# Kernel optimization log

Measured on AMD Instinct MI355X. Metric: run time of the kernel, lower is better.

## Reference

```python
import jax, jax.numpy as jnp
import numpy as np

D_MODEL = 256; H = 8; D_FF = 1024; BLOCKS = 2
NUM_ITEMS = 200000; NUM_USERS = 100000; T_DLT = 512
B = 256; INTER = 50; INTRA = 20; CAND = 2048
NEG_INF = -1e9

def layer_norm(x, g, b, eps=1e-6):
    m = x.mean(-1, keepdims=True)
    s = x.std(-1, keepdims=True, ddof=1)  # torch .std is unbiased
    return g * (x - m) / (s + eps) + b

def pos_encoding(L, d):
    pos = jnp.arange(L, dtype=jnp.float32)[:, None]
    div = jnp.exp(jnp.arange(0, d, 2, dtype=jnp.float32) * (-jnp.log(10000.0) / d))
    pe = jnp.zeros((L, d), dtype=jnp.float32)
    pe = pe.at[:, 0::2].set(jnp.sin(pos * div))
    pe = pe.at[:, 1::2].set(jnp.cos(pos * div))
    return pe

def setup_inputs() -> dict:
    key = jax.random.key(0)
    ks = jax.random.split(key, 20)
    d = D_MODEL
    w = lambda k, shape, s: jax.random.normal(k, shape, dtype=jnp.float32) * s
    s = 1.0 / np.sqrt(d)
    inp = {}
    inp["item_emb"] = w(ks[0], (NUM_ITEMS, d), 0.02)
    inp["user_emb"] = w(ks[1], (NUM_USERS, d), 0.02)
    inp["time_emb"] = w(ks[2], (T_DLT, d), 0.02)
    inp["Wq"] = w(ks[3], (d, d), s); inp["bq"] = jnp.zeros((d,), jnp.float32)
    inp["Wk"] = w(ks[4], (d, d), s); inp["bk"] = jnp.zeros((d,), jnp.float32)
    inp["Wv"] = w(ks[5], (d, d), s); inp["bv"] = jnp.zeros((d,), jnp.float32)
    inp["Wo"] = w(ks[6], (d, d), s); inp["bo"] = jnp.zeros((d,), jnp.float32)
    inp["ln1_g"] = jnp.ones((d,), jnp.float32); inp["ln1_b"] = jnp.zeros((d,), jnp.float32)
    inp["W1"] = w(ks[7], (d, D_FF), s); inp["b1"] = jnp.zeros((D_FF,), jnp.float32)
    inp["W2"] = w(ks[8], (D_FF, d), 1.0 / np.sqrt(D_FF)); inp["b2"] = jnp.zeros((d,), jnp.float32)
    inp["ln2_g"] = jnp.ones((d,), jnp.float32); inp["ln2_b"] = jnp.zeros((d,), jnp.float32)
    inp["fn_g"] = jnp.ones((d,), jnp.float32); inp["fn_b"] = jnp.zeros((d,), jnp.float32)
    inp["gate_Wl"] = w(ks[9], (d, d), s)
    inp["gate_Ws"] = w(ks[10], (d, d), s)
    inp["gate_Wt"] = w(ks[11], (d, d), s)
    inp["gate_bias"] = w(ks[12], (1, d), s)
    inp["batch_us"] = jax.random.randint(ks[13], (B,), 1, NUM_USERS)
    inp["batch_sessions"] = jax.random.randint(ks[14], (B, INTER, INTRA), 0, NUM_ITEMS)
    inp["batch_timedlt"] = jax.random.randint(ks[15], (B,), 0, T_DLT)
    inp["batch_to_predict"] = jax.random.randint(ks[16], (B, CAND), 1, NUM_ITEMS)
    return inp

def reference(item_emb, user_emb, time_emb, Wq, bq, Wk, bk, Wv, bv, Wo, bo,
              ln1_g, ln1_b, W1, b1, W2, b2, ln2_g, ln2_b, fn_g, fn_b,
              gate_Wl, gate_Ws, gate_Wt, gate_bias,
              batch_us, batch_sessions, batch_timedlt, batch_to_predict):
    d = D_MODEL
    item_e = item_emb.at[0].set(0.0)  # padding_idx=0
    user_e = user_emb.at[0].set(0.0)
    E = item_e[batch_sessions]              # [B, INTER, INTRA, d]
    U_embs = user_e[batch_us]               # [B, d]
    t_embs = time_emb[batch_timedlt]        # [B, d]
    Bsz = E.shape[0]
    # intra-session attention (single-head scaled dot-product, padding mask only)
    x = E.reshape(-1, INTRA, d)             # [B*INTER, INTRA, d]
    pad1 = (batch_sessions.reshape(-1, INTRA) != 0)[:, None, :]
    scores = jnp.einsum('nqd,nkd->nqk', x, x) / jnp.sqrt(jnp.float32(d))
    p = jax.nn.softmax(jnp.where(pad1, scores, NEG_INF), axis=-1)
    atted = jnp.einsum('nqk,nkd->nqd', p, x)
    E_hat = atted.sum(axis=1).reshape(Bsz, INTER, d)
    u_short = E_hat[:, -1, :]
    pad2 = (batch_sessions[:, :, 0] != 0)[:, None, None, :]   # [B,1,1,INTER]
    S = E_hat + pos_encoding(INTER, d)[None]
    dh = d // H
    for _ in range(BLOCKS):  # same sublayer applied blocks times (shared weights)
        y = layer_norm(S, ln1_g, ln1_b)
        q = (y @ Wq + bq).reshape(Bsz, INTER, H, dh)
        k = (y @ Wk + bk).reshape(Bsz, INTER, H, dh)
        v = (y @ Wv + bv).reshape(Bsz, INTER, H, dh)
        att = jnp.einsum('bqhe,bkhe->bhqk', q, k) / jnp.sqrt(jnp.float32(dh))
        aw = jax.nn.softmax(jnp.where(pad2, att, NEG_INF), axis=-1)
        o = jnp.einsum('bhqk,bkhe->bqhe', aw, v).reshape(Bsz, INTER, d)
        S = S + o @ Wo + bo
        y2 = layer_norm(S, ln2_g, ln2_b)
        S = S + jax.nn.relu(y2 @ W1 + b1) @ W2 + b2
    S1 = layer_norm(S, fn_g, fn_b)
    u_long = S1.sum(axis=1) + U_embs
    Tg = jax.nn.sigmoid(u_long @ gate_Wl + u_short @ gate_Ws + t_embs @ gate_Wt + gate_bias)
    U = Tg * u_short + (1.0 - Tg) * u_long
    cand = item_e[batch_to_predict]         # [B, CAND, d]
    return jnp.einsum('bcd,bd->bc', cand, U)
```

## Files before the change

### kernel.cpp

```cpp
#include <hip/hip_runtime.h>
#include <math.h>

#define D 256
#define HEADS 8
#define DH 32
#define INTER 50
#define INTRA 20
#define BSZ 256
#define CANDN 2048
#define ROWS (BSZ*INTER)
#define NITEMS 200000

typedef unsigned short ushort_t;
typedef __attribute__((ext_vector_type(8))) short bf16x8;
typedef __attribute__((ext_vector_type(4))) float f32x4;

__device__ __forceinline__ unsigned short f2b(float f) {
    union { float f; unsigned u; } v; v.f = f;
    unsigned r = v.u + 0x7fffu + ((v.u >> 16) & 1u);
    return (unsigned short)(r >> 16);
}
__device__ __forceinline__ float b2f(unsigned short h) {
    union { unsigned u; float f; } v; v.u = ((unsigned)h) << 16;
    return v.f;
}
__device__ __forceinline__ void gl_lds16(const void* g, void* l) {
    __builtin_amdgcn_global_load_lds(
        (const __attribute__((address_space(1))) unsigned int*)g,
        (__attribute__((address_space(3))) unsigned int*)l, 16, 0, 0);
}

__device__ __forceinline__ void wtr_body(const float* __restrict__ W, int K, int N,
    unsigned short* __restrict__ WT, int bx, int by, float (*tile)[33], int t)
{
    int n0 = bx*32, k0 = by*32;
    int tx = t & 31, ty = t >> 5;
    for (int i = ty; i < 32; i += 8)
        tile[i][tx] = W[(size_t)(k0+i)*N + n0 + tx];
    __syncthreads();
    for (int i = ty; i < 32; i += 8)
        WT[(size_t)(n0+i)*K + k0 + tx] = f2b(tile[tx][i]);
}

__global__ __launch_bounds__(256) void prep_k(
    const float* __restrict__ item_emb, unsigned short* __restrict__ item_b, int itemBlocks,
    const float* __restrict__ Wq, const float* __restrict__ Wk,
    const float* __restrict__ Wv, const float* __restrict__ Wo,
    const float* __restrict__ W1, const float* __restrict__ W2,
    unsigned short* __restrict__ WqkvT, unsigned short* __restrict__ WoT,
    unsigned short* __restrict__ W1T, unsigned short* __restrict__ W2T,
    const float* __restrict__ bq, const float* __restrict__ bk,
    const float* __restrict__ bv, float* __restrict__ bqkv)
{
    __shared__ float tile[32][33];
    int blk = blockIdx.x, t = threadIdx.x;
    if (blk < itemBlocks) {
        int i = blk*256 + t;
        float4 v = ((const float4*)item_emb)[i];
        ushort4 h; h.x=f2b(v.x); h.y=f2b(v.y); h.z=f2b(v.z); h.w=f2b(v.w);
        ((ushort4*)item_b)[i] = h;
        return;
    }
    blk -= itemBlocks;
    if (blk < 64)       wtr_body(Wq, 256, 256,  WqkvT,            blk & 7,  blk >> 3, tile, t);
    else if (blk < 128) wtr_body(Wk, 256, 256,  WqkvT + 256*256, (blk-64) & 7,  (blk-64) >> 3, tile, t);
    else if (blk < 192) wtr_body(Wv, 256, 256,  WqkvT + 512*256, (blk-128) & 7, (blk-128) >> 3, tile, t);
    else if (blk < 256) wtr_body(Wo, 256, 256,  WoT,             (blk-192) & 7, (blk-192) >> 3, tile, t);
    else if (blk < 512) { int id = blk-256; wtr_body(W1, 256, 1024, W1T, id & 31, id >> 5, tile, t); }
    else if (blk < 768) { int id = blk-512; wtr_body(W2, 1024, 256, W2T, id & 7,  id >> 3, tile, t); }
    else { bqkv[t] = bq[t]; bqkv[256+t] = bk[t]; bqkv[512+t] = bv[t]; }
}

#define XST 264
__global__ __launch_bounds__(256) void intra_k(
    const float* __restrict__ item_emb, const unsigned short* __restrict__ item_b,
    const int* __restrict__ sess,
    float* __restrict__ S, float* __restrict__ u_short)
{
    __shared__ __align__(16) unsigned short xb[4][INTRA][XST];
    __shared__ __align__(16) unsigned short zrow[XST];
    __shared__ float sc[4][20][21];
    __shared__ float wsum[4][20];
    __shared__ int ids[4][INTRA];
    int t = threadIdx.x, w = t >> 6, lane = t & 63;
    int s = blockIdx.x*4 + w;
    if (lane < INTRA) ids[w][lane] = sess[s*INTRA + lane];
    if (t < 132) ((unsigned int*)zrow)[t] = 0u;
    __syncthreads();
    int col = lane*4;
    for (int r = 0; r < INTRA; ++r) {
        int id = ids[w][r];
        ushort4 h;
        if (id == 0) { h.x=h.y=h.z=h.w=0; }
        else if (item_b) {
            h = *(const ushort4*)(item_b + (size_t)id*D + col);
        } else {
            float4 v4 = *(const float4*)(item_emb + (size_t)id*D + col);
            h.x=f2b(v4.x); h.y=f2b(v4.y); h.z=f2b(v4.z); h.w=f2b(v4.w);
        }
        *(ushort4*)&xb[w][r][col] = h;
    }
    __syncthreads();
    int ml = lane & 15, q8 = (lane >> 4) * 8;
    int r1 = 16 + ml;
    f32x4 acc[2][2] = {};
    for (int k0 = 0; k0 < D; k0 += 32) {
        bf16x8 fr0 = *(const bf16x8*)&xb[w][ml][k0 + q8];
        bf16x8 fr1 = (r1 < INTRA) ? *(const bf16x8*)&xb[w][r1][k0 + q8]
                                  : *(const bf16x8*)&zrow[q8];
        acc[0][0] = __builtin_amdgcn_mfma_f32_16x16x32_bf16(fr0, fr0, acc[0][0], 0,0,0);
        acc[0][1] = __builtin_amdgcn_mfma_f32_16x16x32_bf16(fr0, fr1, acc[0][1], 0,0,0);
        acc[1][0] = __builtin_amdgcn_mfma_f32_16x16x32_bf16(fr1, fr0, acc[1][0], 0,0,0);
        acc[1][1] = __builtin_amdgcn_mfma_f32_16x16x32_bf16(fr1, fr1, acc[1][1], 0,0,0);
    }
    int rb = (lane >> 4) * 4;
    #pragma unroll
    for (int mt = 0; mt < 2; ++mt)
        #pragma unroll
        for (int nt = 0; nt < 2; ++nt)
            #pragma unroll
            for (int i = 0; i < 4; ++i) {
                int row = mt*16 + rb + i, cc = nt*16 + ml;
                if (row < INTRA && cc < INTRA) sc[w][row][cc] = acc[mt][nt][i];
            }
    __syncthreads();
    if (lane < INTRA) {
        float vrow[INTRA]; float mx = -1e30f;
        #pragma unroll
        for (int k = 0; k < INTRA; ++k) {
            float v_ = (ids[w][k] != 0) ? sc[w][lane][k]*(1.0f/16.0f) : -1e9f;
            vrow[k] = v_; mx = fmaxf(mx, v_);
        }
        float ssum = 0.f;
        #pragma unroll
        for (int k = 0; k < INTRA; ++k) { float e_ = expf(vrow[k]-mx); vrow[k]=e_; ssum+=e_; }
        float inv = 1.f/ssum;
        #pragma unroll
        for (int k = 0; k < INTRA; ++k) sc[w][lane][k] = vrow[k]*inv;
    }
    __syncthreads();
    if (lane < INTRA) {
        float s_ = 0.f;
        #pragma unroll
        for (int q = 0; q < INTRA; ++q) s_ += sc[w][q][lane];
        wsum[w][lane] = s_;
    }
    __syncthreads();
    float4 v = {0.f,0.f,0.f,0.f};
    #pragma unroll
    for (int k = 0; k < INTRA; ++k) {
        float ws_ = wsum[w][k];
        ushort4 h = *(const ushort4*)&xb[w][k][col];
        v.x += ws_*b2f(h.x); v.y += ws_*b2f(h.y);
        v.z += ws_*b2f(h.z); v.w += ws_*b2f(h.w);
    }
    int b = s / INTER, srow = s % INTER;
    if (srow == INTER-1) *(float4*)(u_short + (size_t)b*D + col) = v;
    const float kc = -9.210340371976184f / 256.0f;
    float div0 = expf((float)col * kc);
    float div2 = expf((float)(col+2) * kc);
    float4 o;
    o.x = v.x + sinf((float)srow * div0);
    o.y = v.y + cosf((float)srow * div0);
    o.z = v.z + sinf((float)srow * div2);
    o.w = v.w + cosf((float)srow * div2);
    *(float4*)(S + (size_t)s*D + col) = o;
}

__global__ __launch_bounds__(256) void ln4_k(const float* __restrict__ X,
    const float* __restrict__ g, const float* __restrict__ bb,
    unsigned short* __restrict__ Yb, float* __restrict__ Yf)
{
    int w = threadIdx.x >> 6, lane = threadIdx.x & 63;
    size_t row = (size_t)blockIdx.x*4 + w;
    int col = lane*4;
    float4 x = *(const float4*)(X + row*D + col);
    float s_ = x.x + x.y + x.z + x.w;
    #pragma unroll
    for (int off = 32; off > 0; off >>= 1) s_ += __shfl_xor(s_, off, 64);
    float mean = s_ * (1.f/256.f);
    float4 d0; d0.x = x.x-mean; d0.y = x.y-mean; d0.z = x.z-mean; d0.w = x.w-mean;
    float q_ = d0.x*d0.x + d0.y*d0.y + d0.z*d0.z + d0.w*d0.w;
    #pragma unroll
    for (int off = 32; off > 0; off >>= 1) q_ += __shfl_xor(q_, off, 64);
    float inv = 1.f/(sqrtf(q_ * (1.f/255.f)) + 1e-6f);
    float4 g4 = *(const float4*)(g + col), b4 = *(const float4*)(bb + col);
    float4 y;
    y.x = g4.x*d0.x*inv + b4.x; y.y = g4.y*d0.y*inv + b4.y;
    y.z = g4.z*d0.z*inv + b4.z; y.w = g4.w*d0.w*inv + b4.w;
    if (Yb) {
        ushort4 h; h.x=f2b(y.x); h.y=f2b(y.y); h.z=f2b(y.z); h.w=f2b(y.w);
        *(ushort4*)(Yb + row*D + col) = h;
    } else {
        *(float4*)(Yf + row*D + col) = y;
    }
}

#define TM 128
#define TN 128
__global__ __launch_bounds__(256) void mgemm_k(
    const unsigned short* __restrict__ A, int lda,
    const unsigned short* __restrict__ BT,
    const float* __restrict__ bias,
    float* __restrict__ Cf, unsigned short* __restrict__ Cb,
    int ldc, int K, int flags)
{
    __shared__ __align__(16) unsigned short As[2][TM*32];
    __shared__ __align__(16) unsigned short Bs[2][TN*32];
    int tid = threadIdx.x;
    int lane = tid & 63, w = tid >> 6;
    int wrow = (w >> 1) * 64, wcol = (w & 1) * 64;
    int tile_m = blockIdx.y * TM, tile_n = blockIdx.x * TN;
    f32x4 acc[4][4] = {};
    const int r_in_chunk = lane >> 2;
    const int e_in_row = (lane & 3) * 8;
    const int qoff = (lane >> 4) * 8;
    const int ml = lane & 15;
    for (int k0 = 0; k0 < K; k0 += 64) {
        #pragma unroll
        for (int h = 0; h < 2; ++h) {
            #pragma unroll
            for (int i = 0; i < 2; ++i) {
                int c = w*2 + i;
                int row = c*16 + r_in_chunk;
                gl_lds16(A + (size_t)(tile_m + row)*lda + k0 + h*32 + e_in_row,
                         (char*)As[h] + c*1024 + lane*16);
            }
            #pragma unroll
            for (int i = 0; i < 2; ++i) {
                int c = w*2 + i;
                int row = c*16 + r_in_chunk;
                gl_lds16(BT + (size_t)(tile_n + row)*K + k0 + h*32 + e_in_row,
                         (char*)Bs[h] + c*1024 + lane*16);
            }
        }
        __syncthreads();
        #pragma unroll
        for (int h = 0; h < 2; ++h) {
            bf16x8 af[4], bfr[4];
            #pragma unroll
            for (int mt = 0; mt < 4; ++mt)
                af[mt] = *(const bf16x8*)(As[h] + (wrow + mt*16 + ml)*32 + qoff);
            #pragma unroll
            for (int nt = 0; nt < 4; ++nt)
                bfr[nt] = *(const bf16x8*)(Bs[h] + (wcol + nt*16 + ml)*32 + qoff);
            #pragma unroll
            for (int mt = 0; mt < 4; ++mt)
                #pragma unroll
                for (int nt = 0; nt < 4; ++nt)
                    acc[mt][nt] = __builtin_amdgcn_mfma_f32_16x16x32_bf16(
                        af[mt], bfr[nt], acc[mt][nt], 0, 0, 0);
        }
        __syncthreads();
    }
    int col_l = lane & 15, rbase = (lane >> 4) * 4;
    #pragma unroll
    for (int mt = 0; mt < 4; ++mt) {
        #pragma unroll
        for (int nt = 0; nt < 4; ++nt) {
            int col = tile_n + wcol + nt*16 + col_l;
            float bs = bias ? bias[col] : 0.f;
            #pragma unroll
            for (int i = 0; i < 4; ++i) {
                size_t row = tile_m + wrow + mt*16 + rbase + i;
                float v_ = acc[mt][nt][i] + bs;
                if (flags & 2) v_ = fmaxf(v_, 0.f);
                if (flags & 1) Cf[row*ldc + col] += v_;
                else           Cb[row*ldc + col] = f2b(v_);
            }
        }
    }
}

#define AST 40
#define PST 72
__global__ __launch_bounds__(256) void att_k(
    const unsigned short* __restrict__ QKV, const int* __restrict__ sess,
    unsigned short* __restrict__ O)
{
    __shared__ __align__(16) unsigned short qs[64][AST];
    __shared__ __align__(16) unsigned short ks[64][AST];
    __shared__ __align__(16) unsigned short vst[32][PST];
    __shared__ __align__(16) unsigned short pb[64][PST];
    __shared__ float p[50][52];
    __shared__ float msk[52];
    int b = blockIdx.x >> 3, h = blockIdx.x & 7;
    int t = threadIdx.x, w = t >> 6, lane = t & 63;
    for (int u = t; u < 400; u += 256) {
        int arr = u / 200, rem = u % 200, row = rem >> 2, part = rem & 3;
        const unsigned short* src = QKV + ((size_t)(b*INTER+row))*768 + arr*256 + h*32 + part*8;
        ushort4 a = *(const ushort4*)src, c = *(const ushort4*)(src+4);
        unsigned short* dst = (arr ? ks[row] : qs[row]) + part*8;
        *(ushort4*)dst = a; *(ushort4*)(dst+4) = c;
    }
    for (int u = t; u < INTER*32; u += 256) {
        int row = u >> 5, e = u & 31;
        vst[e][row] = QKV[((size_t)(b*INTER+row))*768 + 512 + h*32 + e];
    }
    for (int u = t; u < 32*14; u += 256) {
        int e = u / 14, k = 50 + (u % 14);
        vst[e][k] = 0;
    }
    for (int u = t; u < 64*14; u += 256) {
        int r = u / 14, k = 50 + (u % 14);
        pb[r][k] = 0;
    }
    if (t < INTER) msk[t] = (sess[(b*INTER + t)*INTRA] != 0) ? 1.f : 0.f;
    __syncthreads();
    int ml = lane & 15, q8 = (lane >> 4) * 8, rb = (lane >> 4) * 4;
    {
        bf16x8 afq = *(const bf16x8*)&qs[w*16 + ml][q8];
        #pragma unroll
        for (int nt = 0; nt < 4; ++nt) {
            bf16x8 bfk = *(const bf16x8*)&ks[nt*16 + ml][q8];
            f32x4 a0 = {};
            a0 = __builtin_amdgcn_mfma_f32_16x16x32_bf16(afq, bfk, a0, 0, 0, 0);
            #pragma unroll
            for (int i = 0; i < 4; ++i) {
                int row = w*16 + rb + i, cc = nt*16 + ml;
                if (row < INTER && cc < INTER)
                    p[row][cc] = (msk[cc] != 0.f) ? a0[i]*0.17677669529663687f : -1e9f;
            }
        }
    }
    __syncthreads();
    {
        int r0 = w*13, r1 = r0+13; if (r1 > INTER) r1 = INTER;
        for (int r = r0; r < r1; ++r) {
            float v = (lane < INTER) ? p[r][lane] : -1e30f;
            float m = v;
            #pragma unroll
            for (int off = 32; off > 0; off >>= 1) m = fmaxf(m, __shfl_xor(m, off, 64));
            float e_ = (lane < INTER) ? expf(v - m) : 0.f;
            float ssum = e_;
            #pragma unroll
            for (int off = 32; off > 0; off >>= 1) ssum += __shfl_xor(ssum, off, 64);
            if (lane < INTER) pb[r][lane] = f2b(e_ / ssum);
        }
    }
    __syncthreads();
    f32x4 acco[2] = {};
    #pragma unroll
    for (int kt = 0; kt < 2; ++kt) {
        bf16x8 ap = *(const bf16x8*)&pb[w*16 + ml][kt*32 + q8];
        #pragma unroll
        for (int nt = 0; nt < 2; ++nt) {
            bf16x8 bv = *(const bf16x8*)&vst[nt*16 + ml][kt*32 + q8];
            acco[nt] = __builtin_amdgcn_mfma_f32_16x16x32_bf16(ap, bv, acco[nt], 0, 0, 0);
        }
    }
    #pragma unroll
    for (int nt = 0; nt < 2; ++nt)
        #pragma unroll
        for (int i = 0; i < 4; ++i) {
            int row = w*16 + rb + i, cc = nt*16 + ml;
            if (row < INTER)
                O[((size_t)(b*INTER+row))*D + h*DH + cc] = f2b(acco[nt][i]);
        }
}

__global__ __launch_bounds__(256) void tail_k(
    const float* __restrict__ S,
    const float* __restrict__ fn_g, const float* __restrict__ fn_b,
    const float* __restrict__ user_emb, const int* __restrict__ us,
    const float* __restrict__ time_emb, const int* __restrict__ tdlt,
    const float* __restrict__ u_short,
    const float* __restrict__ Wl, const float* __restrict__ Ws,
    const float* __restrict__ Wt, const float* __restrict__ gb,
    float* __restrict__ U)
{
    __shared__ float part[4][D];
    __shared__ float ul[D], ush[D], te[D];
    int b = blockIdx.x, t = threadIdx.x, w = t >> 6, lane = t & 63;
    int col = lane*4;
    float4 g4 = *(const float4*)(fn_g + col);
    float4 b4 = *(const float4*)(fn_b + col);
    float4 acc4 = {0.f,0.f,0.f,0.f};
    for (int l = w; l < INTER; l += 4) {
        float4 x = *(const float4*)(S + (size_t)(b*INTER + l)*D + col);
        float s = x.x + x.y + x.z + x.w;
        #pragma unroll
        for (int o = 32; o > 0; o >>= 1) s += __shfl_xor(s, o, 64);
        float mean = s * (1.f/256.f);
        float dx = x.x - mean, dy = x.y - mean, dz = x.z - mean, dw = x.w - mean;
        float q = dx*dx + dy*dy + dz*dz + dw*dw;
        #pragma unroll
        for (int o = 32; o > 0; o >>= 1) q += __shfl_xor(q, o, 64);
        float inv = 1.f/(sqrtf(q*(1.f/255.f)) + 1e-6f);
        acc4.x += g4.x*dx*inv + b4.x;
        acc4.y += g4.y*dy*inv + b4.y;
        acc4.z += g4.z*dz*inv + b4.z;
        acc4.w += g4.w*dw*inv + b4.w;
    }
    *(float4*)&part[w][col] = acc4;
    __syncthreads();
    int id = us[b];
    float ue = (id == 0) ? 0.f : user_emb[(size_t)id*D + t];
    float ulv = part[0][t] + part[1][t] + part[2][t] + part[3][t] + ue;
    ul[t]  = ulv;
    float ushv = u_short[b*D + t];
    ush[t] = ushv;
    te[t]  = time_emb[(size_t)tdlt[b]*D + t];
    __syncthreads();
    float a = gb[t];
    for (int k = 0; k < D; ++k)
        a += ul[k]*Wl[k*D + t] + ush[k]*Ws[k*D + t] + te[k]*Wt[k*D + t];
    float tg = 1.f/(1.f + expf(-a));
    U[b*D + t] = tg*ushv + (1.f - tg)*ulv;
}

__global__ __launch_bounds__(256) void out_k(
    const float* __restrict__ item_emb, const unsigned short* __restrict__ item_b,
    const int* __restrict__ pred,
    const float* __restrict__ U, float* __restrict__ out)
{
    int b = blockIdx.x >> 6;
    int cbase = (blockIdx.x & 63) * 32;
    int t = threadIdx.x, w = t >> 6, lane = t & 63;
    int hl = lane & 31, half = lane >> 5;
    float4 u0 = *(const float4*)(U + (size_t)b*D + hl*8);
    float4 u1 = *(const float4*)(U + (size_t)b*D + hl*8 + 4);
    for (int it = 0; it < 4; ++it) {
        int c = cbase + it*8 + w*2 + half;
        int id = pred[b*CANDN + c];
        float p = 0.f;
        if (id) {
            if (item_b) {
                const unsigned short* row = item_b + (size_t)id*D + hl*8;
                ushort4 a = *(const ushort4*)row;
                ushort4 d = *(const ushort4*)(row+4);
                p = b2f(a.x)*u0.x + b2f(a.y)*u0.y + b2f(a.z)*u0.z + b2f(a.w)*u0.w
                  + b2f(d.x)*u1.x + b2f(d.y)*u1.y + b2f(d.z)*u1.z + b2f(d.w)*u1.w;
            } else {
                const float* row = item_emb + (size_t)id*D + hl*8;
                float4 a = *(const float4*)row;
                float4 d = *(const float4*)(row+4);
                p = a.x*u0.x + a.y*u0.y + a.z*u0.z + a.w*u0.w
                  + d.x*u1.x + d.y*u1.y + d.z*u1.z + d.w*u1.w;
            }
        }
        #pragma unroll
        for (int off = 16; off > 0; off >>= 1) p += __shfl_xor(p, off, 64);
        if (hl == 0) out[b*CANDN + c] = p;
    }
}

extern "C" void kernel_launch(void* const* d_in, const int* in_sizes, int n_in,
                              void* d_out, int out_size, void* d_ws, size_t ws_size,
                              hipStream_t stream)
{
    const float* item_emb = (const float*)d_in[0];
    const float* user_emb = (const float*)d_in[1];
    const float* time_emb = (const float*)d_in[2];
    const float* Wq = (const float*)d_in[3];  const float* bq = (const float*)d_in[4];
    const float* Wk = (const float*)d_in[5];  const float* bk = (const float*)d_in[6];
    const float* Wv = (const float*)d_in[7];  const float* bv = (const float*)d_in[8];
    const float* Wo = (const float*)d_in[9];  const float* bo = (const float*)d_in[10];
    const float* ln1_g = (const float*)d_in[11]; const float* ln1_b = (const float*)d_in[12];
    const float* W1 = (const float*)d_in[13]; const float* b1 = (const float*)d_in[14];
    const float* W2 = (const float*)d_in[15]; const float* b2 = (const float*)d_in[16];
    const float* ln2_g = (const float*)d_in[17]; const float* ln2_b = (const float*)d_in[18];
    const float* fn_g = (const float*)d_in[19]; const float* fn_b = (const float*)d_in[20];
    const float* gWl = (const float*)d_in[21]; const float* gWs = (const float*)d_in[22];
    const float* gWt = (const float*)d_in[23]; const float* gbias = (const float*)d_in[24];
    const int* us   = (const int*)d_in[25];
    const int* sess = (const int*)d_in[26];
    const int* tdlt = (const int*)d_in[27];
    const int* pred = (const int*)d_in[28];
    float* out = (float*)d_out;

    char* base = (char*)d_ws;
    size_t off = 0;
    float* S = (float*)(base+off);              off += (size_t)ROWS*D*4;
    unsigned short* Ybf = (unsigned short*)(base+off); off += (size_t)ROWS*D*2;
    unsigned short* QKVb = (unsigned short*)(base+off);
    unsigned short* Hb = QKVb;
    off += (size_t)ROWS*1024*2;
    unsigned short* WqkvT = (unsigned short*)(base+off); off += (size_t)768*256*2;
    unsigned short* WoT   = (unsigned short*)(base+off); off += (size_t)256*256*2;
    unsigned short* W1T   = (unsigned short*)(base+off); off += (size_t)1024*256*2;
    unsigned short* W2T   = (unsigned short*)(base+off); off += (size_t)256*1024*2;
    float* bqkv = (float*)(base+off);            off += 768*4;
    float* u_short = (float*)(base+off);         off += BSZ*D*4;
    float* u_long  = (float*)(base+off);         off += BSZ*D*4;
    float* Ufin    = (float*)(base+off);         off += BSZ*D*4;
    (void)u_long;
    unsigned short* item_b = (unsigned short*)(base+off);
    size_t item_b_bytes = (size_t)NITEMS*D*2;
    bool use_b16 = (off + item_b_bytes) <= ws_size;
    if (!use_b16) item_b = nullptr;

    int itemBlocks = use_b16 ? (NITEMS*D/4)/256 : 0;
    prep_k<<<itemBlocks + 769, 256, 0, stream>>>(
        item_emb, item_b, itemBlocks,
        Wq, Wk, Wv, Wo, W1, W2,
        WqkvT, WoT, W1T, W2T,
        bq, bk, bv, bqkv);

    intra_k<<<ROWS/4, 256, 0, stream>>>(item_emb, item_b, sess, S, u_short);

    for (int blk = 0; blk < 2; ++blk) {
        ln4_k<<<ROWS/4, 256, 0, stream>>>(S, ln1_g, ln1_b, Ybf, nullptr);
        mgemm_k<<<dim3(6,100), 256, 0, stream>>>(Ybf, D, WqkvT, bqkv,
                                                 nullptr, QKVb, 768, 256, 0);
        att_k<<<BSZ*HEADS, 256, 0, stream>>>(QKVb, sess, Ybf);
        mgemm_k<<<dim3(2,100), 256, 0, stream>>>(Ybf, D, WoT, bo,
                                                 S, nullptr, 256, 256, 1);
        ln4_k<<<ROWS/4, 256, 0, stream>>>(S, ln2_g, ln2_b, Ybf, nullptr);
        mgemm_k<<<dim3(8,100), 256, 0, stream>>>(Ybf, D, W1T, b1,
                                                 nullptr, Hb, 1024, 256, 2);
        mgemm_k<<<dim3(2,100), 256, 0, stream>>>(Hb, 1024, W2T, b2,
                                                 S, nullptr, 256, 1024, 1);
    }

    tail_k<<<BSZ, 256, 0, stream>>>(S, fn_g, fn_b, user_emb, us,
        time_emb, tdlt, u_short, gWl, gWs, gWt, gbias, Ufin);

    out_k<<<(BSZ*CANDN)/32, 256, 0, stream>>>(item_emb, item_b, pred, Ufin, out);
}
```

Baseline: 837.7 us.

## Fuse each transformer sublayer into one per-sequence kernel with LDS-resident activations

Replaces the seven-kernel chain per block (two layernorms, four GEMMs, attention) with a single block_k kernel. Each workgroup of 512 threads owns one sequence of 50 rows and keeps the QKV, attention, FFN hidden and residual state in about 150 KB of LDS. Weights are read directly from global memory by every workgroup. This removes launch overhead and the global round-trips of intermediate activations. In exchange there are only 256 workgroups with one per CU due to the LDS footprint, 64-row tiles padded from 50 waste MFMA work, and weight reloads no longer use the shared-memory staging of the old GEMM.

New measurement: 677.4 us. -19.1%, faster.

```diff
diff --git a/kernel.cpp b/kernel.cpp
--- a/kernel.cpp
+++ b/kernel.cpp
@@ -23,11 +23,6 @@
 __device__ __forceinline__ float b2f(unsigned short h) {
     union { unsigned u; float f; } v; v.u = ((unsigned)h) << 16;
     return v.f;
-}
-__device__ __forceinline__ void gl_lds16(const void* g, void* l) {
-    __builtin_amdgcn_global_load_lds(
-        (const __attribute__((address_space(1))) unsigned int*)g,
-        (__attribute__((address_space(3))) unsigned int*)l, 16, 0, 0);
 }
 
 __device__ __forceinline__ void wtr_body(const float* __restrict__ W, int K, int N,
@@ -167,196 +162,330 @@
     *(float4*)(S + (size_t)s*D + col) = o;
 }
 
-__global__ __launch_bounds__(256) void ln4_k(const float* __restrict__ X,
-    const float* __restrict__ g, const float* __restrict__ bb,
-    unsigned short* __restrict__ Yb, float* __restrict__ Yf)
+#define LB_VT 0
+#define LB_Y 36864
+#define LB_Q 70656
+#define LB_K 104448
+#define LB_PB 36864
+#define LB_O 110592
+#define LB_SL 0
+#define LB_Y2 52000
+#define LB_H 85792
+#define LB_MSK 152352
+#define MFMA16(a,b,c) __builtin_amdgcn_mfma_f32_16x16x32_bf16(a, b, c, 0, 0, 0)
+
+__global__ __launch_bounds__(512) void block_k(
+    float* __restrict__ S,
+    const unsigned short* __restrict__ WqkvT, const float* __restrict__ bqkv,
+    const unsigned short* __restrict__ WoT, const float* __restrict__ bo,
+    const unsigned short* __restrict__ W1T, const float* __restrict__ b1,
+    const unsigned short* __restrict__ W2T, const float* __restrict__ b2,
+    const float* __restrict__ ln1_g, const float* __restrict__ ln1_b,
+    const float* __restrict__ ln2_g, const float* __restrict__ ln2_b,
+    const int* __restrict__ sess)
 {
-    int w = threadIdx.x >> 6, lane = threadIdx.x & 63;
-    size_t row = (size_t)blockIdx.x*4 + w;
-    int col = lane*4;
-    float4 x = *(const float4*)(X + row*D + col);
-    float s_ = x.x + x.y + x.z + x.w;
+    __shared__ __align__(16) char LB[152608];
+    unsigned short* Yp  = (unsigned short*)(LB + LB_Y);
+    unsigned short* Qp  = (unsigned short*)(LB + LB_Q);
+    unsigned short* Kp  = (unsigned short*)(LB + LB_K);
+    unsigned short* VTp = (unsigned short*)(LB + LB_VT);
+    unsigned short* Op  = (unsigned short*)(LB + LB_O);
+    unsigned short* Y2p = (unsigned short*)(LB + LB_Y2);
+    unsigned short* Hp  = (unsigned short*)(LB + LB_H);
+    float* Slp  = (float*)(LB + LB_SL);
+    float* mskp = (float*)(LB + LB_MSK);
+
+    int b = blockIdx.x;
+    int t = threadIdx.x, w = t >> 6, lane = t & 63;
+    int ml = lane & 15, q8 = (lane >> 4) * 8;
+    int col_l = ml, rbase = (lane >> 4) * 4;
+    float* Sg = S + (size_t)b * INTER * D;
+
+    if (t < 64) mskp[t] = (t < 50 && sess[(b*INTER + t)*INTRA] != 0) ? 1.f : 0.f;
+    for (int u = t; u < 14*256; u += 512) {
+        int r = 50 + (u >> 8), c = u & 255;
+        Yp[r*264 + c] = 0; Qp[r*264 + c] = 0; Kp[r*264 + c] = 0;
+    }
+    for (int u = t; u < 8*32*14; u += 512) {
+        int hh = u / 448, rem = u % 448;
+        VTp[(hh*32 + rem/14)*72 + 50 + rem%14] = 0;
+    }
+    {
+        int col = lane*4;
+        float4 g4 = *(const float4*)(ln1_g + col), b4 = *(const float4*)(ln1_b + col);
+        for (int r = w; r < 50; r += 8) {
+            float4 x = *(const float4*)(Sg + r*256 + col);
+            float s_ = x.x + x.y + x.z + x.w;
+            #pragma unroll
+            for (int o = 32; o > 0; o >>= 1) s_ += __shfl_xor(s_, o, 64);
+            float mean = s_ * (1.f/256.f);
+            float dx = x.x-mean, dy = x.y-mean, dz = x.z-mean, dw = x.w-mean;
+            float qq = dx*dx + dy*dy + dz*dz + dw*dw;
+            #pragma unroll
+            for (int o = 32; o > 0; o >>= 1) qq += __shfl_xor(qq, o, 64);
+            float inv = 1.f/(sqrtf(qq*(1.f/255.f)) + 1e-6f);
+            ushort4 h;
+            h.x = f2b(g4.x*dx*inv + b4.x); h.y = f2b(g4.y*dy*inv + b4.y);
+            h.z = f2b(g4.z*dz*inv + b4.z); h.w = f2b(g4.w*dw*inv + b4.w);
+            *(ushort4*)&Yp[r*264 + col] = h;
+        }
+    }
+    __syncthreads();
+
+    {
+        f32x4 acc[4][6] = {};
+        #pragma unroll
+        for (int ks = 0; ks < 8; ++ks) {
+            bf16x8 af[4];
+            #pragma unroll
+            for (int mt = 0; mt < 4; ++mt)
+                af[mt] = *(const bf16x8*)&Yp[(mt*16+ml)*264 + ks*32 + q8];
+            bf16x8 bfr[6];
+            #pragma unroll
+            for (int j = 0; j < 6; ++j) {
+                int n = (w*6 + j)*16 + ml;
+                bfr[j] = *(const bf16x8*)(WqkvT + (size_t)n*256 + ks*32 + q8);
+            }
+            #pragma unroll
+            for (int j = 0; j < 6; ++j)
+                #pragma unroll
+                for (int mt = 0; mt < 4; ++mt)
+                    acc[mt][j] = MFMA16(af[mt], bfr[j], acc[mt][j]);
+        }
+        #pragma unroll
+        for (int j = 0; j < 6; ++j) {
+            int n = (w*6 + j)*16 + col_l;
+            float bs = bqkv[n];
+            #pragma unroll
+            for (int mt = 0; mt < 4; ++mt)
+                #pragma unroll
+                for (int i = 0; i < 4; ++i) {
+                    int row = mt*16 + rbase + i;
+                    if (row < 50) {
+                        unsigned short hv = f2b(acc[mt][j][i] + bs);
+                        if (n < 256)      Qp[row*264 + n] = hv;
+                        else if (n < 512) Kp[row*264 + (n-256)] = hv;
+                        else { int hh=(n-512)>>5, e=(n-512)&31; VTp[(hh*32+e)*72 + row] = hv; }
+                    }
+                }
+        }
+    }
+    __syncthreads();
+
+    unsigned short* pbw = (unsigned short*)(LB + LB_PB + w*9216);
+    {
+        f32x4 p3[4][4] = {};
+        {
+            bf16x8 af[4], bf_[4];
+            #pragma unroll
+            for (int mt = 0; mt < 4; ++mt)
+                af[mt] = *(const bf16x8*)&Qp[(mt*16+ml)*264 + w*32 + q8];
+            #pragma unroll
+            for (int nt = 0; nt < 4; ++nt)
+                bf_[nt] = *(const bf16x8*)&Kp[(nt*16+ml)*264 + w*32 + q8];
+            #pragma unroll
+            for (int mt = 0; mt < 4; ++mt)
+                #pragma unroll
+                for (int nt = 0; nt < 4; ++nt)
+                    p3[mt][nt] = MFMA16(af[mt], bf_[nt], p3[mt][nt]);
+        }
+        float mk[4];
+        #pragma unroll
+        for (int nt = 0; nt < 4; ++nt) mk[nt] = mskp[nt*16 + ml];
+        __syncthreads();
+        #pragma unroll
+        for (int mt = 0; mt < 4; ++mt)
+            #pragma unroll
+            for (int i = 0; i < 4; ++i) {
+                int row = mt*16 + rbase + i;
+                float v[4]; float m = -1e30f;
+                #pragma unroll
+                for (int nt = 0; nt < 4; ++nt) {
+                    float x = (mk[nt] != 0.f) ? p3[mt][nt][i]*0.17677669529663687f : -1e9f;
+                    v[nt] = x; m = fmaxf(m, x);
+                }
+                #pragma unroll
+                for (int o = 8; o > 0; o >>= 1) m = fmaxf(m, __shfl_xor(m, o, 64));
+                float s_ = 0.f;
+                #pragma unroll
+                for (int nt = 0; nt < 4; ++nt) { v[nt] = expf(v[nt] - m); s_ += v[nt]; }
+                #pragma unroll
+                for (int o = 8; o > 0; o >>= 1) s_ += __shfl_xor(s_, o, 64);
+                float inv = 1.f / s_;
+                if (row < 50) {
+                    #pragma unroll
+                    for (int nt = 0; nt < 4; ++nt)
+                        pbw[row*72 + nt*16 + ml] = f2b(v[nt]*inv);
+                }
+            }
+    }
+    {
+        f32x4 po[4][2] = {};
+        #pragma unroll
+        for (int kt = 0; kt < 2; ++kt) {
+            bf16x8 af[4], bv_[2];
+            #pragma unroll
+            for (int mt = 0; mt < 4; ++mt)
+                af[mt] = *(const bf16x8*)&pbw[(mt*16+ml)*72 + kt*32 + q8];
+            #pragma unroll
+            for (int nt = 0; nt < 2; ++nt)
+                bv_[nt] = *(const bf16x8*)&VTp[(w*32 + nt*16 + ml)*72 + kt*32 + q8];
+            #pragma unroll
+            for (int nt = 0; nt < 2; ++nt)
+                #pragma unroll
+                for (int mt = 0; mt < 4; ++mt)
+                    po[mt][nt] = MFMA16(af[mt], bv_[nt], po[mt][nt]);
+        }
+        #pragma unroll
+        for (int nt = 0; nt < 2; ++nt)
+            #pragma unroll
+            for (int mt = 0; mt < 4; ++mt)
+                #pragma unroll
+                for (int i = 0; i < 4; ++i) {
+                    int row = mt*16 + rbase + i;
+                    if (row < 50)
+                        Op[row*264 + w*32 + nt*16 + col_l] = f2b(po[mt][nt][i]);
+                }
+    }
+    __syncthreads();
+
+    {
+        f32x4 a5[4][2] = {};
+        #pragma unroll
+        for (int ks = 0; ks < 8; ++ks) {
+            bf16x8 af[4], bw[2];
+            #pragma unroll
+            for (int mt = 0; mt < 4; ++mt)
+                af[mt] = *(const bf16x8*)&Op[(mt*16+ml)*264 + ks*32 + q8];
+            #pragma unroll
+            for (int j = 0; j < 2; ++j) {
+                int n = w*32 + j*16 + ml;
+                bw[j] = *(const bf16x8*)(WoT + (size_t)n*256 + ks*32 + q8);
+            }
+            #pragma unroll
+            for (int j = 0; j < 2; ++j)
+                #pragma unroll
+                for (int mt = 0; mt < 4; ++mt)
+                    a5[mt][j] = MFMA16(af[mt], bw[j], a5[mt][j]);
+        }
+        #pragma unroll
+        for (int j = 0; j < 2; ++j) {
+            int n = w*32 + j*16 + col_l;
+            float bv = bo[n];
+            #pragma unroll
+            for (int mt = 0; mt < 4; ++mt)
+                #pragma unroll
+                for (int i = 0; i < 4; ++i) {
+                    int row = mt*16 + rbase + i;
+                    if (row < 50)
+                        Slp[row*260 + n] = Sg[row*256 + n] + a5[mt][j][i] + bv;
+                }
+        }
+    }
+    __syncthreads();
+
+    {
+        int col = lane*4;
+        float4 g4 = *(const float4*)(ln2_g + col), b4 = *(const float4*)(ln2_b + col);
+        for (int r = w; r < 50; r += 8) {
+            float4 x = *(const float4*)&Slp[r*260 + col];
+            float s_ = x.x + x.y + x.z + x.w;
+            #pragma unroll
+            for (int o = 32; o > 0; o >>= 1) s_ += __shfl_xor(s_, o, 64);
+            float mean = s_ * (1.f/256.f);
+            float dx = x.x-mean, dy = x.y-mean, dz = x.z-mean, dw = x.w-mean;
+            float qq = dx*dx + dy*dy + dz*dz + dw*dw;
+            #pragma unroll
+            for (int o = 32; o > 0; o >>= 1) qq += __shfl_xor(qq, o, 64);
+            float inv = 1.f/(sqrtf(qq*(1.f/255.f)) + 1e-6f);
+            ushort4 h;
+            h.x = f2b(g4.x*dx*inv + b4.x); h.y = f2b(g4.y*dy*inv + b4.y);
+            h.z = f2b(g4.z*dz*inv + b4.z); h.w = f2b(g4.w*dw*inv + b4.w);
+            *(ushort4*)&Y2p[r*264 + col] = h;
+        }
+        for (int u = t; u < 14*256; u += 512) {
+            int r = 50 + (u >> 8), c = u & 255;
+            Y2p[r*264 + c] = 0;
+        }
+    }
+    __syncthreads();
+
     #pragma unroll
-    for (int off = 32; off > 0; off >>= 1) s_ += __shfl_xor(s_, off, 64);
-    float mean = s_ * (1.f/256.f);
-    float4 d0; d0.x = x.x-mean; d0.y = x.y-mean; d0.z = x.z-mean; d0.w = x.w-mean;
-    float q_ = d0.x*d0.x + d0.y*d0.y + d0.z*d0.z + d0.w*d0.w;
-    #pragma unroll
-    for (int off = 32; off > 0; off >>= 1) q_ += __shfl_xor(q_, off, 64);
-    float inv = 1.f/(sqrtf(q_ * (1.f/255.f)) + 1e-6f);
-    float4 g4 = *(const float4*)(g + col), b4 = *(const float4*)(bb + col);
-    float4 y;
-    y.x = g4.x*d0.x*inv + b4.x; y.y = g4.y*d0.y*inv + b4.y;
-    y.z = g4.z*d0.z*inv + b4.z; y.w = g4.w*d0.w*inv + b4.w;
-    if (Yb) {
-        ushort4 h; h.x=f2b(y.x); h.y=f2b(y.y); h.z=f2b(y.z); h.w=f2b(y.w);
-        *(ushort4*)(Yb + row*D + col) = h;
-    } else {
-        *(float4*)(Yf + row*D + col) = y;
-    }
-}
-
-#define TM 128
-#define TN 128
-__global__ __launch_bounds__(256) void mgemm_k(
-    const unsigned short* __restrict__ A, int lda,
-    const unsigned short* __restrict__ BT,
-    const float* __restrict__ bias,
-    float* __restrict__ Cf, unsigned short* __restrict__ Cb,
-    int ldc, int K, int flags)
-{
-    __shared__ __align__(16) unsigned short As[2][TM*32];
-    __shared__ __align__(16) unsigned short Bs[2][TN*32];
-    int tid = threadIdx.x;
-    int lane = tid & 63, w = tid >> 6;
-    int wrow = (w >> 1) * 64, wcol = (w & 1) * 64;
-    int tile_m = blockIdx.y * TM, tile_n = blockIdx.x * TN;
-    f32x4 acc[4][4] = {};
-    const int r_in_chunk = lane >> 2;
-    const int e_in_row = (lane & 3) * 8;
-    const int qoff = (lane >> 4) * 8;
-    const int ml = lane & 15;
-    for (int k0 = 0; k0 < K; k0 += 64) {
-        #pragma unroll
-        for (int h = 0; h < 2; ++h) {
-            #pragma unroll
-            for (int i = 0; i < 2; ++i) {
-                int c = w*2 + i;
-                int row = c*16 + r_in_chunk;
-                gl_lds16(A + (size_t)(tile_m + row)*lda + k0 + h*32 + e_in_row,
-                         (char*)As[h] + c*1024 + lane*16);
-            }
-            #pragma unroll
-            for (int i = 0; i < 2; ++i) {
-                int c = w*2 + i;
-                int row = c*16 + r_in_chunk;
-                gl_lds16(BT + (size_t)(tile_n + row)*K + k0 + h*32 + e_in_row,
-                         (char*)Bs[h] + c*1024 + lane*16);
+    for (int hf = 0; hf < 2; ++hf) {
+        {
+            f32x4 a7[4][4] = {};
+            #pragma unroll
+            for (int ks = 0; ks < 8; ++ks) {
+                bf16x8 af[4], bw[4];
+                #pragma unroll
+                for (int mt = 0; mt < 4; ++mt)
+                    af[mt] = *(const bf16x8*)&Y2p[(mt*16+ml)*264 + ks*32 + q8];
+                #pragma unroll
+                for (int j = 0; j < 4; ++j) {
+                    int n = hf*512 + w*64 + j*16 + ml;
+                    bw[j] = *(const bf16x8*)(W1T + (size_t)n*256 + ks*32 + q8);
+                }
+                #pragma unroll
+                for (int j = 0; j < 4; ++j)
+                    #pragma unroll
+                    for (int mt = 0; mt < 4; ++mt)
+                        a7[mt][j] = MFMA16(af[mt], bw[j], a7[mt][j]);
+            }
+            #pragma unroll
+            for (int j = 0; j < 4; ++j) {
+                int nl = w*64 + j*16 + col_l;
+                float bv = b1[hf*512 + nl];
+                #pragma unroll
+                for (int mt = 0; mt < 4; ++mt)
+                    #pragma unroll
+                    for (int i = 0; i < 4; ++i) {
+                        int row = mt*16 + rbase + i;
+                        if (row < 50)
+                            Hp[row*520 + nl] = f2b(fmaxf(a7[mt][j][i] + bv, 0.f));
+                    }
             }
         }
         __syncthreads();
-        #pragma unroll
-        for (int h = 0; h < 2; ++h) {
-            bf16x8 af[4], bfr[4];
-            #pragma unroll
-            for (int mt = 0; mt < 4; ++mt)
-                af[mt] = *(const bf16x8*)(As[h] + (wrow + mt*16 + ml)*32 + qoff);
-            #pragma unroll
-            for (int nt = 0; nt < 4; ++nt)
-                bfr[nt] = *(const bf16x8*)(Bs[h] + (wcol + nt*16 + ml)*32 + qoff);
-            #pragma unroll
-            for (int mt = 0; mt < 4; ++mt)
-                #pragma unroll
-                for (int nt = 0; nt < 4; ++nt)
-                    acc[mt][nt] = __builtin_amdgcn_mfma_f32_16x16x32_bf16(
-                        af[mt], bfr[nt], acc[mt][nt], 0, 0, 0);
+        {
+            f32x4 a8[4][2] = {};
+            #pragma unroll
+            for (int ks = 0; ks < 16; ++ks) {
+                bf16x8 af[4], bw[2];
+                #pragma unroll
+                for (int mt = 0; mt < 4; ++mt)
+                    af[mt] = *(const bf16x8*)&Hp[(mt*16+ml)*520 + ks*32 + q8];
+                #pragma unroll
+                for (int j = 0; j < 2; ++j) {
+                    int n = w*32 + j*16 + ml;
+                    bw[j] = *(const bf16x8*)(W2T + (size_t)n*1024 + hf*512 + ks*32 + q8);
+                }
+                #pragma unroll
+                for (int j = 0; j < 2; ++j)
+                    #pragma unroll
+                    for (int mt = 0; mt < 4; ++mt)
+                        a8[mt][j] = MFMA16(af[mt], bw[j], a8[mt][j]);
+            }
+            #pragma unroll
+            for (int j = 0; j < 2; ++j) {
+                int n = w*32 + j*16 + col_l;
+                float bv = (hf == 0) ? b2[n] : 0.f;
+                #pragma unroll
+                for (int mt = 0; mt < 4; ++mt)
+                    #pragma unroll
+                    for (int i = 0; i < 4; ++i) {
+                        int row = mt*16 + rbase + i;
+                        if (row < 50)
+                            Slp[row*260 + n] += a8[mt][j][i] + bv;
+                    }
+            }
         }
         __syncthreads();
     }
-    int col_l = lane & 15, rbase = (lane >> 4) * 4;
-    #pragma unroll
-    for (int mt = 0; mt < 4; ++mt) {
-        #pragma unroll
-        for (int nt = 0; nt < 4; ++nt) {
-            int col = tile_n + wcol + nt*16 + col_l;
-            float bs = bias ? bias[col] : 0.f;
-            #pragma unroll
-            for (int i = 0; i < 4; ++i) {
-                size_t row = tile_m + wrow + mt*16 + rbase + i;
-                float v_ = acc[mt][nt][i] + bs;
-                if (flags & 2) v_ = fmaxf(v_, 0.f);
-                if (flags & 1) Cf[row*ldc + col] += v_;
-                else           Cb[row*ldc + col] = f2b(v_);
-            }
-        }
-    }
-}
-
-#define AST 40
-#define PST 72
-__global__ __launch_bounds__(256) void att_k(
-    const unsigned short* __restrict__ QKV, const int* __restrict__ sess,
-    unsigned short* __restrict__ O)
-{
-    __shared__ __align__(16) unsigned short qs[64][AST];
-    __shared__ __align__(16) unsigned short ks[64][AST];
-    __shared__ __align__(16) unsigned short vst[32][PST];
-    __shared__ __align__(16) unsigned short pb[64][PST];
-    __shared__ float p[50][52];
-    __shared__ float msk[52];
-    int b = blockIdx.x >> 3, h = blockIdx.x & 7;
-    int t = threadIdx.x, w = t >> 6, lane = t & 63;
-    for (int u = t; u < 400; u += 256) {
-        int arr = u / 200, rem = u % 200, row = rem >> 2, part = rem & 3;
-        const unsigned short* src = QKV + ((size_t)(b*INTER+row))*768 + arr*256 + h*32 + part*8;
-        ushort4 a = *(const ushort4*)src, c = *(const ushort4*)(src+4);
-        unsigned short* dst = (arr ? ks[row] : qs[row]) + part*8;
-        *(ushort4*)dst = a; *(ushort4*)(dst+4) = c;
-    }
-    for (int u = t; u < INTER*32; u += 256) {
-        int row = u >> 5, e = u & 31;
-        vst[e][row] = QKV[((size_t)(b*INTER+row))*768 + 512 + h*32 + e];
-    }
-    for (int u = t; u < 32*14; u += 256) {
-        int e = u / 14, k = 50 + (u % 14);
-        vst[e][k] = 0;
-    }
-    for (int u = t; u < 64*14; u += 256) {
-        int r = u / 14, k = 50 + (u % 14);
-        pb[r][k] = 0;
-    }
-    if (t < INTER) msk[t] = (sess[(b*INTER + t)*INTRA] != 0) ? 1.f : 0.f;
-    __syncthreads();
-    int ml = lane & 15, q8 = (lane >> 4) * 8, rb = (lane >> 4) * 4;
-    {
-        bf16x8 afq = *(const bf16x8*)&qs[w*16 + ml][q8];
-        #pragma unroll
-        for (int nt = 0; nt < 4; ++nt) {
-            bf16x8 bfk = *(const bf16x8*)&ks[nt*16 + ml][q8];
-            f32x4 a0 = {};
-            a0 = __builtin_amdgcn_mfma_f32_16x16x32_bf16(afq, bfk, a0, 0, 0, 0);
-            #pragma unroll
-            for (int i = 0; i < 4; ++i) {
-                int row = w*16 + rb + i, cc = nt*16 + ml;
-                if (row < INTER && cc < INTER)
-                    p[row][cc] = (msk[cc] != 0.f) ? a0[i]*0.17677669529663687f : -1e9f;
-            }
-        }
-    }
-    __syncthreads();
-    {
-        int r0 = w*13, r1 = r0+13; if (r1 > INTER) r1 = INTER;
-        for (int r = r0; r < r1; ++r) {
-            float v = (lane < INTER) ? p[r][lane] : -1e30f;
-            float m = v;
-            #pragma unroll
-            for (int off = 32; off > 0; off >>= 1) m = fmaxf(m, __shfl_xor(m, off, 64));
-            float e_ = (lane < INTER) ? expf(v - m) : 0.f;
-            float ssum = e_;
-            #pragma unroll
-            for (int off = 32; off > 0; off >>= 1) ssum += __shfl_xor(ssum, off, 64);
-            if (lane < INTER) pb[r][lane] = f2b(e_ / ssum);
-        }
-    }
-    __syncthreads();
-    f32x4 acco[2] = {};
-    #pragma unroll
-    for (int kt = 0; kt < 2; ++kt) {
-        bf16x8 ap = *(const bf16x8*)&pb[w*16 + ml][kt*32 + q8];
-        #pragma unroll
-        for (int nt = 0; nt < 2; ++nt) {
-            bf16x8 bv = *(const bf16x8*)&vst[nt*16 + ml][kt*32 + q8];
-            acco[nt] = __builtin_amdgcn_mfma_f32_16x16x32_bf16(ap, bv, acco[nt], 0, 0, 0);
-        }
-    }
-    #pragma unroll
-    for (int nt = 0; nt < 2; ++nt)
-        #pragma unroll
-        for (int i = 0; i < 4; ++i) {
-            int row = w*16 + rb + i, cc = nt*16 + ml;
-            if (row < INTER)
-                O[((size_t)(b*INTER+row))*D + h*DH + cc] = f2b(acco[nt][i]);
-        }
+
+    for (int u = t; u < 50*256; u += 512) {
+        int r = u >> 8, c = u & 255;
+        Sg[r*256 + c] = Slp[r*260 + c];
+    }
 }
 
 __global__ __launch_bounds__(256) void tail_k(
@@ -472,19 +601,13 @@
     char* base = (char*)d_ws;
     size_t off = 0;
     float* S = (float*)(base+off);              off += (size_t)ROWS*D*4;
-    unsigned short* Ybf = (unsigned short*)(base+off); off += (size_t)ROWS*D*2;
-    unsigned short* QKVb = (unsigned short*)(base+off);
-    unsigned short* Hb = QKVb;
-    off += (size_t)ROWS*1024*2;
     unsigned short* WqkvT = (unsigned short*)(base+off); off += (size_t)768*256*2;
     unsigned short* WoT   = (unsigned short*)(base+off); off += (size_t)256*256*2;
     unsigned short* W1T   = (unsigned short*)(base+off); off += (size_t)1024*256*2;
     unsigned short* W2T   = (unsigned short*)(base+off); off += (size_t)256*1024*2;
     float* bqkv = (float*)(base+off);            off += 768*4;
     float* u_short = (float*)(base+off);         off += BSZ*D*4;
-    float* u_long  = (float*)(base+off);         off += BSZ*D*4;
     float* Ufin    = (float*)(base+off);         off += BSZ*D*4;
-    (void)u_long;
     unsigned short* item_b = (unsigned short*)(base+off);
     size_t item_b_bytes = (size_t)NITEMS*D*2;
     bool use_b16 = (off + item_b_bytes) <= ws_size;
@@ -499,19 +622,10 @@
 
     intra_k<<<ROWS/4, 256, 0, stream>>>(item_emb, item_b, sess, S, u_short);
 
-    for (int blk = 0; blk < 2; ++blk) {
-        ln4_k<<<ROWS/4, 256, 0, stream>>>(S, ln1_g, ln1_b, Ybf, nullptr);
-        mgemm_k<<<dim3(6,100), 256, 0, stream>>>(Ybf, D, WqkvT, bqkv,
-                                                 nullptr, QKVb, 768, 256, 0);
-        att_k<<<BSZ*HEADS, 256, 0, stream>>>(QKVb, sess, Ybf);
-        mgemm_k<<<dim3(2,100), 256, 0, stream>>>(Ybf, D, WoT, bo,
-                                                 S, nullptr, 256, 256, 1);
-        ln4_k<<<ROWS/4, 256, 0, stream>>>(S, ln2_g, ln2_b, Ybf, nullptr);
-        mgemm_k<<<dim3(8,100), 256, 0, stream>>>(Ybf, D, W1T, b1,
-                                                 nullptr, Hb, 1024, 256, 2);
-        mgemm_k<<<dim3(2,100), 256, 0, stream>>>(Hb, 1024, W2T, b2,
-                                                 S, nullptr, 256, 1024, 1);
-    }
+    for (int blk = 0; blk < 2; ++blk)
+        block_k<<<BSZ, 512, 0, stream>>>(S, WqkvT, bqkv, WoT, bo,
+                                         W1T, b1, W2T, b2,
+                                         ln1_g, ln1_b, ln2_g, ln2_b, sess);
 
     tail_k<<<BSZ, 256, 0, stream>>>(S, fn_g, fn_b, user_emb, us,
         time_emb, tdlt, u_short, gWl, gWs, gWt, gbias, Ufin);
```
